# Kernel optimization log

Hardware: AMD Instinct MI355X
Metric: run time of the kernel (lower is better)

## Reference

```python
import jax, jax.numpy as jnp
from jax import lax
import numpy as np


def _edt_to(zero_mask):
    """Exact Euclidean distance from every pixel to the nearest True pixel of
    zero_mask. Equivalent to scipy.ndimage.distance_transform_edt(~zero_mask).
    Separable two-pass algorithm: 1-D distance along W (two scans), then an
    exact lower-envelope min along H using squared distances.
    zero_mask: bool [B, H, W] -> float32 [B, H, W].
    """
    B, H, W = zero_mask.shape
    INF = jnp.float32(H + W)  # larger than any attainable 1-D distance
    bg = jnp.transpose(zero_mask, (2, 0, 1))  # [W, B, H]: scan over W

    def step(c, b):
        c = jnp.where(b, 0.0, c + 1.0)
        return c, c

    init = jnp.full((B, H), INF, dtype=jnp.float32)
    _, f = lax.scan(step, init, bg)                 # left-to-right
    _, r = lax.scan(step, init, bg, reverse=True)   # right-to-left
    d1 = jnp.minimum(f, r)                          # [W, B, H] 1-D dist along W
    g = jnp.transpose(d1 * d1, (1, 2, 0))           # [B, H, W] squared 1-D dist

    # d2[b, y, x] = min_{y'} g[b, y', x] + (y - y')^2   (exact 2-D squared EDT)
    yy = jnp.arange(H, dtype=jnp.float32)
    dy2 = (yy[:, None] - yy[None, :]) ** 2          # [H, H']
    d2 = jnp.min(g[:, None, :, :] + dy2[None, :, :, None], axis=2)  # [B, H, W]
    return jnp.sqrt(d2)


def _boundary_loss(preds, targets, idx_class=None):
    B, C, H, W = preds.shape
    probs = jax.nn.softmax(preds, axis=1)
    classes = [idx_class] if idx_class is not None else list(range(1, C))
    total = jnp.float32(0.0)
    count = jnp.float32(0.0)
    for cls in classes:
        pos = targets == cls        # bool [B, H, W]
        neg = ~pos
        has = jnp.any(pos)
        # scipy: distance(negmask)*negmask - (distance(posmask)-1)*posmask
        # distance_transform_edt(negmask) == dist to nearest pos pixel, etc.
        dmap = _edt_to(pos) * neg - (_edt_to(neg) - 1.0) * pos
        loss = jnp.mean(dmap * probs[:, cls])
        total = total + jnp.where(has, loss, 0.0)
        count = count + has.astype(jnp.float32)
    return jnp.where(count > 0, total / jnp.maximum(count, 1.0), jnp.float32(0.0))


def setup_inputs() -> dict:
    key = jax.random.key(0)
    k1, k2 = jax.random.split(key)
    preds = jax.random.normal(k1, (8, 4, 256, 256), dtype=jnp.float32)
    targets = jax.random.randint(k2, (8, 256, 256), 0, 4)
    return {"preds": preds, "targets": targets}


def reference(preds, targets):
    return _boundary_loss(preds, targets, idx_class=None)
```

## Files before the change

kernel.cpp:

```cpp
#include <hip/hip_runtime.h>
#include <math.h>

#define BB 8
#define HH 256
#define WW 256
#define T  2
#define NW 4

typedef unsigned long long u64;

__global__ __launch_bounds__(256) void build_masks(const int* __restrict__ tgt,
                                                   u64* __restrict__ masks) {
  const int x = threadIdx.x;
  const int b = blockIdx.x;
  const int w = blockIdx.y;
  u64 m0 = 0, m1 = 0, m2 = 0, m3 = 0, bit = 1ull;
  const int* p = tgt + ((size_t)b * HH + w * 64) * WW + x;
  for (int ly = 0; ly < 64; ++ly, bit += bit) {
    int e = p[ly * WW];
    m0 |= (e == 0) ? bit : 0ull;
    m1 |= (e == 1) ? bit : 0ull;
    m2 |= (e == 2) ? bit : 0ull;
    m3 |= (e == 3) ? bit : 0ull;
  }
  const size_t base = (size_t)b * 4 * NW * WW + (size_t)w * WW + x;
  masks[base + 0 * NW * WW] = m0;
  masks[base + 1 * NW * WW] = m1;
  masks[base + 2 * NW * WW] = m2;
  masks[base + 3 * NW * WW] = m3;
}

__global__ __launch_bounds__(256, 2) void fused(const u64* __restrict__ masks,
                                                const int* __restrict__ tgt,
                                                const float* __restrict__ preds,
                                                float* __restrict__ out) {
  __shared__ float g[T][WW][4];
  __shared__ int   wred[4];
  __shared__ float fred[4];
  const int x  = threadIdx.x;
  const int b  = blockIdx.x;
  const int y0 = blockIdx.y * T;
  const int wy = y0 >> 6;

  u64 m[4][NW];
#pragma unroll
  for (int k = 0; k < 4; ++k)
#pragma unroll
    for (int w = 0; w < NW; ++w)
      m[k][w] = masks[(((size_t)b * 4 + k) * NW + w) * WW + x];

  int lmax = 0;
#pragma unroll
  for (int j = 0; j < T; ++j) {
    const int y  = y0 + j;
    const int ly = y & 63;
    const int ini = min(513 + y, 768 - y);
    float4 gv;
    float* gp = (float*)&gv;
#pragma unroll
    for (int k = 0; k < 4; ++k) {
      int best = ini;
#pragma unroll
      for (int w = 0; w < NW; ++w) {
        u64 bits = m[k][w];
        if (w < wy) {
          int d = y - (w * 64 + 63 - __clzll((long long)bits));
          best = min(best, bits ? d : 1024);
        } else if (w > wy) {
          int d = w * 64 + (__ffsll((long long)bits) - 1) - y;
          best = min(best, bits ? d : 1024);
        } else {
          u64 lo = bits & ((2ull << ly) - 1ull);
          u64 hi = bits >> ly;
          int dl = ly - 63 + __clzll((long long)lo);
          int dh = __ffsll((long long)hi) - 1;
          best = min(best, lo ? dl : 1024);
          best = min(best, hi ? dh : 1024);
        }
      }
      lmax = max(lmax, best);
      gp[k] = (float)(best * best);
    }
    *(float4*)&g[j][x][0] = gv;
  }

#pragma unroll
  for (int off = 32; off; off >>= 1) lmax = max(lmax, __shfl_xor(lmax, off, 64));
  if ((x & 63) == 0) wred[x >> 6] = lmax;
  __syncthreads();
  const int R = max(max(wred[0], wred[1]), max(wred[2], wred[3]));

  float acc = 0.0f;
#pragma unroll
  for (int j = 0; j < T; ++j) {
    const int y = y0 + j;
    float d0 = 1e30f, d1 = 1e30f, d2 = 1e30f, d3 = 1e30f;
#pragma unroll 4
    for (int kk = -R; kk <= R; ++kk) {
      int xp = min(max(x + kk, 0), WW - 1);
      float dx  = (float)(x - xp);
      float dx2 = dx * dx;
      float4 gv = *(const float4*)&g[j][xp][0];
      d0 = fminf(d0, gv.x + dx2);
      d1 = fminf(d1, gv.y + dx2);
      d2 = fminf(d2, gv.z + dx2);
      d3 = fminf(d3, gv.w + dx2);
    }

    const int t = tgt[((size_t)b * HH + y) * WW + x];
    const float* pb = preds + ((size_t)b * 4 * HH + y) * WW + x;
    float p0 = pb[0 * HH * WW], p1 = pb[1 * HH * WW];
    float p2 = pb[2 * HH * WW], p3 = pb[3 * HH * WW];
    float pm = fmaxf(fmaxf(p0, p1), fmaxf(p2, p3));
    float e0 = expf(p0 - pm), e1 = expf(p1 - pm);
    float e2 = expf(p2 - pm), e3 = expf(p3 - pm);
    float inv = 1.0f / (e0 + e1 + e2 + e3);

    float dn1 = fminf(d0, fminf(d2, d3));
    float dn2 = fminf(d0, fminf(d1, d3));
    float dn3 = fminf(d0, fminf(d1, d2));
    float c1 = (t == 1) ? (1.0f - sqrtf(dn1)) : sqrtf(d1);
    float c2 = (t == 2) ? (1.0f - sqrtf(dn2)) : sqrtf(d2);
    float c3 = (t == 3) ? (1.0f - sqrtf(dn3)) : sqrtf(d3);
    acc += (c1 * e1 + c2 * e2 + c3 * e3) * inv;
  }

#pragma unroll
  for (int off = 32; off; off >>= 1) acc += __shfl_down(acc, off, 64);
  if ((x & 63) == 0) fred[x >> 6] = acc;
  __syncthreads();
  if (x == 0)
    atomicAdd(out, (fred[0] + fred[1] + fred[2] + fred[3]) *
                       (1.0f / (3.0f * BB * HH * WW)));
}

extern "C" void kernel_launch(void* const* d_in, const int* in_sizes, int n_in,
                              void* d_out, int out_size, void* d_ws, size_t ws_size,
                              hipStream_t stream) {
  const float* preds = (const float*)d_in[0];
  const int*   tgt   = (const int*)d_in[1];
  float* out   = (float*)d_out;
  u64*   masks = (u64*)d_ws;

  hipMemsetAsync(out, 0, sizeof(float), stream);
  build_masks<<<dim3(BB, NW), 256, 0, stream>>>(tgt, masks);
  fused<<<dim3(BB, HH / T), 256, 0, stream>>>(masks, tgt, preds, out);
}
```

Measured before the change: 88.37 us.

## Use per-wave search radius, padded LDS rows and symmetric window scan

The horizontal min-plus pass now bounds its search radius per wavefront instead of per block. Each lane's own squared distance already caps its answer, so this stays exact while letting waves with small distances stop early. Row buffers in shared memory get padding filled with large sentinels, so the scan drops index clamping and checks both ±k neighbours in one step. A clamped fallback loop covers radii larger than the padding. The output memset is folded into the mask-building kernel and the occupancy hint is raised, at the cost of extra LDS for the padding.

```diff
diff --git a/kernel.cpp b/kernel.cpp
--- a/kernel.cpp
+++ b/kernel.cpp
@@ -6,14 +6,18 @@
 #define WW 256
 #define T  2
 #define NW 4
+#define PAD 96
+#define LDSW (WW + 2 * PAD)
 
 typedef unsigned long long u64;
 
 __global__ __launch_bounds__(256) void build_masks(const int* __restrict__ tgt,
-                                                   u64* __restrict__ masks) {
+                                                   u64* __restrict__ masks,
+                                                   float* __restrict__ out) {
   const int x = threadIdx.x;
   const int b = blockIdx.x;
   const int w = blockIdx.y;
+  if (b == 0 && w == 0 && x == 0) out[0] = 0.0f;
   u64 m0 = 0, m1 = 0, m2 = 0, m3 = 0, bit = 1ull;
   const int* p = tgt + ((size_t)b * HH + w * 64) * WW + x;
   for (int ly = 0; ly < 64; ++ly, bit += bit) {
@@ -30,17 +34,23 @@
   masks[base + 3 * NW * WW] = m3;
 }
 
-__global__ __launch_bounds__(256, 2) void fused(const u64* __restrict__ masks,
+__global__ __launch_bounds__(256, 4) void fused(const u64* __restrict__ masks,
                                                 const int* __restrict__ tgt,
                                                 const float* __restrict__ preds,
                                                 float* __restrict__ out) {
-  __shared__ float g[T][WW][4];
-  __shared__ int   wred[4];
+  __shared__ float g[T][LDSW][4];
   __shared__ float fred[4];
   const int x  = threadIdx.x;
   const int b  = blockIdx.x;
   const int y0 = blockIdx.y * T;
   const int wy = y0 >> 6;
+
+  for (int i = x; i < T * 2 * PAD; i += 256) {
+    int j = i / (2 * PAD);
+    int q = i - j * (2 * PAD);
+    int idx = (q < PAD) ? q : (q + WW);
+    *(float4*)&g[j][idx][0] = make_float4(1e30f, 1e30f, 1e30f, 1e30f);
+  }
 
   u64 m[4][NW];
 #pragma unroll
@@ -81,32 +91,57 @@
       lmax = max(lmax, best);
       gp[k] = (float)(best * best);
     }
-    *(float4*)&g[j][x][0] = gv;
+    *(float4*)&g[j][x + PAD][0] = gv;
   }
 
 #pragma unroll
   for (int off = 32; off; off >>= 1) lmax = max(lmax, __shfl_xor(lmax, off, 64));
-  if ((x & 63) == 0) wred[x >> 6] = lmax;
+  const int R  = __builtin_amdgcn_readfirstlane(lmax);
+  const int Rw = min(R, PAD);
   __syncthreads();
-  const int R = max(max(wred[0], wred[1]), max(wred[2], wred[3]));
+
+  float d[T][4];
+#pragma unroll
+  for (int j = 0; j < T; ++j) {
+    float4 own = *(const float4*)&g[j][x + PAD][0];
+    d[j][0] = own.x; d[j][1] = own.y; d[j][2] = own.z; d[j][3] = own.w;
+  }
+
+  for (int kk = 1; kk <= Rw; ++kk) {
+    float fkk = (float)kk;
+    float fk2 = fkk * fkk;
+#pragma unroll
+    for (int j = 0; j < T; ++j) {
+      float4 gm = *(const float4*)&g[j][x + PAD - kk][0];
+      float4 gp = *(const float4*)&g[j][x + PAD + kk][0];
+      d[j][0] = fminf(d[j][0], fminf(gm.x, gp.x) + fk2);
+      d[j][1] = fminf(d[j][1], fminf(gm.y, gp.y) + fk2);
+      d[j][2] = fminf(d[j][2], fminf(gm.z, gp.z) + fk2);
+      d[j][3] = fminf(d[j][3], fminf(gm.w, gp.w) + fk2);
+    }
+  }
+  if (R > PAD) {
+#pragma unroll 1
+    for (int kk = PAD + 1; kk <= R; ++kk) {
+      int xm = max(x - kk, 0), xp = min(x + kk, WW - 1);
+      float dm = (float)(x - xm), dpq = (float)(xp - x);
+      float dm2 = dm * dm, dp2 = dpq * dpq;
+#pragma unroll
+      for (int j = 0; j < T; ++j) {
+        float4 gm = *(const float4*)&g[j][xm + PAD][0];
+        float4 gp = *(const float4*)&g[j][xp + PAD][0];
+        d[j][0] = fminf(d[j][0], fminf(gm.x + dm2, gp.x + dp2));
+        d[j][1] = fminf(d[j][1], fminf(gm.y + dm2, gp.y + dp2));
+        d[j][2] = fminf(d[j][2], fminf(gm.z + dm2, gp.z + dp2));
+        d[j][3] = fminf(d[j][3], fminf(gm.w + dm2, gp.w + dp2));
+      }
+    }
+  }
 
   float acc = 0.0f;
 #pragma unroll
   for (int j = 0; j < T; ++j) {
     const int y = y0 + j;
-    float d0 = 1e30f, d1 = 1e30f, d2 = 1e30f, d3 = 1e30f;
-#pragma unroll 4
-    for (int kk = -R; kk <= R; ++kk) {
-      int xp = min(max(x + kk, 0), WW - 1);
-      float dx  = (float)(x - xp);
-      float dx2 = dx * dx;
-      float4 gv = *(const float4*)&g[j][xp][0];
-      d0 = fminf(d0, gv.x + dx2);
-      d1 = fminf(d1, gv.y + dx2);
-      d2 = fminf(d2, gv.z + dx2);
-      d3 = fminf(d3, gv.w + dx2);
-    }
-
     const int t = tgt[((size_t)b * HH + y) * WW + x];
     const float* pb = preds + ((size_t)b * 4 * HH + y) * WW + x;
     float p0 = pb[0 * HH * WW], p1 = pb[1 * HH * WW];
@@ -116,12 +151,12 @@
     float e2 = expf(p2 - pm), e3 = expf(p3 - pm);
     float inv = 1.0f / (e0 + e1 + e2 + e3);
 
-    float dn1 = fminf(d0, fminf(d2, d3));
-    float dn2 = fminf(d0, fminf(d1, d3));
-    float dn3 = fminf(d0, fminf(d1, d2));
-    float c1 = (t == 1) ? (1.0f - sqrtf(dn1)) : sqrtf(d1);
-    float c2 = (t == 2) ? (1.0f - sqrtf(dn2)) : sqrtf(d2);
-    float c3 = (t == 3) ? (1.0f - sqrtf(dn3)) : sqrtf(d3);
+    float dn1 = fminf(d[j][0], fminf(d[j][2], d[j][3]));
+    float dn2 = fminf(d[j][0], fminf(d[j][1], d[j][3]));
+    float dn3 = fminf(d[j][0], fminf(d[j][1], d[j][2]));
+    float c1 = (t == 1) ? (1.0f - sqrtf(dn1)) : sqrtf(d[j][1]);
+    float c2 = (t == 2) ? (1.0f - sqrtf(dn2)) : sqrtf(d[j][2]);
+    float c3 = (t == 3) ? (1.0f - sqrtf(dn3)) : sqrtf(d[j][3]);
     acc += (c1 * e1 + c2 * e2 + c3 * e3) * inv;
   }
 
@@ -142,7 +177,6 @@
   float* out   = (float*)d_out;
   u64*   masks = (u64*)d_ws;
 
-  hipMemsetAsync(out, 0, sizeof(float), stream);
-  build_masks<<<dim3(BB, NW), 256, 0, stream>>>(tgt, masks);
+  build_masks<<<dim3(BB, NW), 256, 0, stream>>>(tgt, masks, out);
   fused<<<dim3(BB, HH / T), 256, 0, stream>>>(masks, tgt, preds, out);
 }
```

After: 85.63 us. -3.1%, faster.
